# Kernel tuning notes

Measured on AMD Instinct MI355X. Metric: run time of the kernel, lower is better.

The kernel has to match this reference:

```python
import jax, jax.numpy as jnp
import numpy as np

EPS = 1e-08


def squash(x):
    # x: [..., D]; scale by ||x||^2/(1+||x||^2) and normalize by ||x||
    lengths2 = jnp.sum(x * x, axis=-1, keepdims=True)
    lengths = jnp.sqrt(lengths2)
    return x * (lengths2 / (1.0 + lengths2)) / (lengths + EPS)


def setup_inputs() -> dict:
    key = jax.random.key(0)
    k1, = jax.random.split(key, 1)
    B, G, S, O, D = 32, 8, 1152, 10, 16
    u_predict = jax.random.normal(k1, (B, G, S, O, D), dtype=jnp.float32)
    b_param = jnp.zeros((G, 1, S, O), dtype=jnp.float32)
    return {"u_predict": u_predict, "b_param": b_param, "n_iterations": 3}


def reference(u_predict, b_param, n_iterations):
    B, G, S, O, D = u_predict.shape
    # b: expand param (G,1,S,O) -> (G,B,S,O), permute -> (B,G,S,O)
    b = jnp.transpose(jnp.broadcast_to(b_param, (G, B, S, O)), (1, 0, 2, 3))
    v = None
    for r in range(n_iterations):
        c = jax.nn.softmax(b, axis=3)[..., None]          # [B,G,S,O,1]
        s = jnp.sum(c * u_predict, axis=2)                # [B,G,O,D]
        v = squash(s)                                     # [B,G,O,D]
        if r < n_iterations - 1:
            # agreement: dot(u_predict, v) over D
            b = b + jnp.sum(u_predict * v[:, :, None], axis=-1)  # [B,G,S,O]
    return jnp.sum(v, axis=1)                             # [B,O,D]
```

## Files before the change

### kernel.cpp

```cpp
#include <hip/hip_runtime.h>
#include <hip/hip_fp16.h>
#include <stdint.h>

#define NB 32
#define NG 8
#define NS 1152
#define NO 10
#define ND 16
#define EPSV 1e-8f

#define THREADS 512
#define GRPS (THREADS / 4)
#define NSTEPS (NS / GRPS)
#define UHROW (NO * 4)

typedef float f4v __attribute__((ext_vector_type(4)));

__global__ __launch_bounds__(THREADS)
void AgreementRouting_72988674228343_kernel(const float* __restrict__ u,
                                            const float* __restrict__ bparam,
                                            const int* __restrict__ n_iter_p,
                                            float* __restrict__ out,
                                            uint2* __restrict__ uh)
{
    __shared__ float  b_lds[NS * NO];
    __shared__ float4 sred[8][NO][4];
    __shared__ float4 v_lds[NO][4];

    const int tid  = threadIdx.x;
    const int bg   = blockIdx.x;
    const int g    = bg & 7;
    const int bb   = bg >> 3;
    const int wave = tid >> 6;
    const int lane = tid & 63;
    const int d4   = tid & 3;
    const int grp  = tid >> 2;

    const int n = n_iter_p[0];

    const float* bp = bparam + (size_t)g * (NS * NO);
    for (int i = tid; i < NS * NO; i += THREADS) b_lds[i] = bp[i];
    if (tid < NO * 4) v_lds[tid >> 2][tid & 3] = make_float4(0.f, 0.f, 0.f, 0.f);

    const f4v* ub  = (const f4v*)u + (size_t)bg * (NS * NO * 4);
    uint2*     uhb = uh + (size_t)bg * (NS * UHROW);

    __syncthreads();

    for (int r = 0; r < n; ++r) {
        float4 sacc[NO];
#pragma unroll
        for (int o = 0; o < NO; ++o) sacc[o] = make_float4(0.f, 0.f, 0.f, 0.f);

        for (int step = 0; step < NSTEPS; ++step) {
            const int s = step * GRPS + grp;
            float4 uu[NO];
            float bnew[NO];

            if (r == 0) {
                const f4v* row = ub + (size_t)s * (NO * 4) + d4;
                f4v t[NO];
#pragma unroll
                for (int o = 0; o < NO; ++o) t[o] = __builtin_nontemporal_load(row + o * 4);
                if (n > 1) {
                    uint2* wrow = uhb + (size_t)s * UHROW + d4;
#pragma unroll
                    for (int o = 0; o < NO; ++o) {
                        const __half2 lo = __floats2half2_rn(t[o].x, t[o].y);
                        const __half2 hi = __floats2half2_rn(t[o].z, t[o].w);
                        uint2 pk;
                        pk.x = __builtin_bit_cast(uint32_t, lo);
                        pk.y = __builtin_bit_cast(uint32_t, hi);
                        wrow[o * 4] = pk;
                    }
                }
#pragma unroll
                for (int o = 0; o < NO; ++o) {
                    uu[o] = make_float4(t[o].x, t[o].y, t[o].z, t[o].w);
                    bnew[o] = b_lds[s * NO + o];
                }
            } else {
                const uint2* row = uhb + (size_t)s * UHROW + d4;
                uint2 pk[NO];
#pragma unroll
                for (int o = 0; o < NO; ++o) pk[o] = row[o * 4];
#pragma unroll
                for (int o = 0; o < NO; ++o) {
                    const float2 a = __half22float2(__builtin_bit_cast(__half2, pk[o].x));
                    const float2 b = __half22float2(__builtin_bit_cast(__half2, pk[o].y));
                    uu[o] = make_float4(a.x, a.y, b.x, b.y);
                }
#pragma unroll
                for (int o = 0; o < NO; ++o) {
                    const float4 vc = v_lds[o][d4];
                    float p = uu[o].x * vc.x + uu[o].y * vc.y +
                              uu[o].z * vc.z + uu[o].w * vc.w;
                    p += __shfl_xor(p, 1);
                    p += __shfl_xor(p, 2);
                    bnew[o] = b_lds[s * NO + o] + p;
                }
            }

            float mx = bnew[0];
#pragma unroll
            for (int o = 1; o < NO; ++o) mx = fmaxf(mx, bnew[o]);
            float ss = 0.f;
#pragma unroll
            for (int o = 0; o < NO; ++o) { bnew[o] = __expf(bnew[o] - mx); ss += bnew[o]; }
            const float inv = 1.f / ss;
#pragma unroll
            for (int o = 0; o < NO; ++o) {
                const float c = bnew[o] * inv;
                sacc[o].x += c * uu[o].x;
                sacc[o].y += c * uu[o].y;
                sacc[o].z += c * uu[o].z;
                sacc[o].w += c * uu[o].w;
            }
        }

#pragma unroll
        for (int o = 0; o < NO; ++o) {
#pragma unroll
            for (int mask = 4; mask <= 32; mask <<= 1) {
                sacc[o].x += __shfl_xor(sacc[o].x, mask);
                sacc[o].y += __shfl_xor(sacc[o].y, mask);
                sacc[o].z += __shfl_xor(sacc[o].z, mask);
                sacc[o].w += __shfl_xor(sacc[o].w, mask);
            }
        }
        if (lane < 4) {
#pragma unroll
            for (int o = 0; o < NO; ++o) sred[wave][o][lane] = sacc[o];
        }
        __syncthreads();

        if (tid < NO * 4) {
            const int o = tid >> 2, dd = tid & 3;
            float4 sv = sred[0][o][dd];
#pragma unroll
            for (int w = 1; w < 8; ++w) {
                const float4 t = sred[w][o][dd];
                sv.x += t.x; sv.y += t.y; sv.z += t.z; sv.w += t.w;
            }
            float q = sv.x * sv.x + sv.y * sv.y + sv.z * sv.z + sv.w * sv.w;
            q += __shfl_xor(q, 1);
            q += __shfl_xor(q, 2);
            const float len = sqrtf(q);
            const float f = (q / (1.f + q)) / (len + EPSV);
            const float4 vv = make_float4(sv.x * f, sv.y * f, sv.z * f, sv.w * f);
            const float4 c4 = v_lds[o][dd];
            v_lds[o][dd] = make_float4(c4.x + vv.x, c4.y + vv.y,
                                       c4.z + vv.z, c4.w + vv.w);
            if (r == n - 1) {
                float* op = out + (size_t)bb * (NO * ND) + o * ND + dd * 4;
                atomicAdd(op + 0, vv.x);
                atomicAdd(op + 1, vv.y);
                atomicAdd(op + 2, vv.z);
                atomicAdd(op + 3, vv.w);
            }
        }
        __syncthreads();
    }
}

extern "C" void kernel_launch(void* const* d_in, const int* in_sizes, int n_in,
                              void* d_out, int out_size, void* d_ws, size_t ws_size,
                              hipStream_t stream) {
    const float* u   = (const float*)d_in[0];
    const float* bp  = (const float*)d_in[1];
    const int*   nit = (const int*)d_in[2];
    float* out = (float*)d_out;
    uint2* uh  = (uint2*)d_ws;

    hipMemsetAsync(out, 0, (size_t)out_size * sizeof(float), stream);

    AgreementRouting_72988674228343_kernel<<<dim3(NB * NG), dim3(THREADS), 0, stream>>>(
        u, bp, nit, out, uh);
}
```

Before: 313.2 us.

## Remap thread-to-data layout to 8-element chunks and software-prefetch fp16 rows

Each of the 4 threads per capsule row now owns contiguous 8-float chunks covering half of an output's D dimension for alternating outputs, instead of 4 floats across all 10 outputs. This lets the fp16 cache be written and read with 16-byte uint4 accesses and cuts shuffle traffic for the dot products. Later iterations fully unroll the S loop with double-buffered prefetch of the next row's loads, and v is held in registers. The cost is higher register pressure from the 5x8 accumulators, the prefetch buffers and the v copy, which may reduce occupancy.

```diff
diff --git a/kernel.cpp b/kernel.cpp
--- a/kernel.cpp
+++ b/kernel.cpp
@@ -10,9 +10,7 @@
 #define EPSV 1e-8f
 
 #define THREADS 512
-#define GRPS (THREADS / 4)
-#define NSTEPS (NS / GRPS)
-#define UHROW (NO * 4)
+#define NSTEPS 9
 
 typedef float f4v __attribute__((ext_vector_type(4)));
 
@@ -21,11 +19,11 @@
                                             const float* __restrict__ bparam,
                                             const int* __restrict__ n_iter_p,
                                             float* __restrict__ out,
-                                            uint2* __restrict__ uh)
+                                            uint4* __restrict__ uh)
 {
-    __shared__ float  b_lds[NS * NO];
-    __shared__ float4 sred[8][NO][4];
-    __shared__ float4 v_lds[NO][4];
+    __shared__ float b_lds[NS * NO];
+    __shared__ float sredl[8][4][5][8];
+    __shared__ float v_lds[NO * ND];
 
     const int tid  = threadIdx.x;
     const int bg   = blockIdx.x;
@@ -33,131 +31,162 @@
     const int bb   = bg >> 3;
     const int wave = tid >> 6;
     const int lane = tid & 63;
-    const int d4   = tid & 3;
-    const int grp  = tid >> 2;
+    const int j    = tid & 3;
+    const int rl   = tid >> 2;
+    const int half8 = j & 1;
+    const int par   = j >> 1;
 
     const int n = n_iter_p[0];
 
     const float* bp = bparam + (size_t)g * (NS * NO);
     for (int i = tid; i < NS * NO; i += THREADS) b_lds[i] = bp[i];
-    if (tid < NO * 4) v_lds[tid >> 2][tid & 3] = make_float4(0.f, 0.f, 0.f, 0.f);
-
-    const f4v* ub  = (const f4v*)u + (size_t)bg * (NS * NO * 4);
-    uint2*     uhb = uh + (size_t)bg * (NS * UHROW);
+    if (tid < NO * ND) v_lds[tid] = 0.f;
+
+    const f4v* u4  = (const f4v*)u + (size_t)bg * (NS * 40);
+    uint4*     uh4 = uh + (size_t)bg * (NS * 20);
 
     __syncthreads();
 
     for (int r = 0; r < n; ++r) {
-        float4 sacc[NO];
-#pragma unroll
-        for (int o = 0; o < NO; ++o) sacc[o] = make_float4(0.f, 0.f, 0.f, 0.f);
-
-        for (int step = 0; step < NSTEPS; ++step) {
-            const int s = step * GRPS + grp;
-            float4 uu[NO];
-            float bnew[NO];
-
-            if (r == 0) {
-                const f4v* row = ub + (size_t)s * (NO * 4) + d4;
-                f4v t[NO];
-#pragma unroll
-                for (int o = 0; o < NO; ++o) t[o] = __builtin_nontemporal_load(row + o * 4);
-                if (n > 1) {
-                    uint2* wrow = uhb + (size_t)s * UHROW + d4;
-#pragma unroll
-                    for (int o = 0; o < NO; ++o) {
-                        const __half2 lo = __floats2half2_rn(t[o].x, t[o].y);
-                        const __half2 hi = __floats2half2_rn(t[o].z, t[o].w);
-                        uint2 pk;
-                        pk.x = __builtin_bit_cast(uint32_t, lo);
-                        pk.y = __builtin_bit_cast(uint32_t, hi);
-                        wrow[o * 4] = pk;
+        float sacc[5][8];
+#pragma unroll
+        for (int k = 0; k < 5; ++k)
+#pragma unroll
+            for (int i = 0; i < 8; ++i) sacc[k][i] = 0.f;
+
+        if (r == 0) {
+            for (int step = 0; step < NSTEPS; ++step) {
+                const int s = step * 128 + rl;
+                float uf[5][8];
+#pragma unroll
+                for (int k = 0; k < 5; ++k) {
+                    const int f = k * 4 + j;
+                    const f4v a = __builtin_nontemporal_load(u4 + (size_t)s * 40 + f * 2);
+                    const f4v b = __builtin_nontemporal_load(u4 + (size_t)s * 40 + f * 2 + 1);
+                    uf[k][0] = a.x; uf[k][1] = a.y; uf[k][2] = a.z; uf[k][3] = a.w;
+                    uf[k][4] = b.x; uf[k][5] = b.y; uf[k][6] = b.z; uf[k][7] = b.w;
+                    if (n > 1) {
+                        uint4 pk;
+                        pk.x = __builtin_bit_cast(uint32_t, __floats2half2_rn(a.x, a.y));
+                        pk.y = __builtin_bit_cast(uint32_t, __floats2half2_rn(a.z, a.w));
+                        pk.z = __builtin_bit_cast(uint32_t, __floats2half2_rn(b.x, b.y));
+                        pk.w = __builtin_bit_cast(uint32_t, __floats2half2_rn(b.z, b.w));
+                        uh4[(size_t)s * 20 + f] = pk;
                     }
                 }
-#pragma unroll
-                for (int o = 0; o < NO; ++o) {
-                    uu[o] = make_float4(t[o].x, t[o].y, t[o].z, t[o].w);
-                    bnew[o] = b_lds[s * NO + o];
-                }
-            } else {
-                const uint2* row = uhb + (size_t)s * UHROW + d4;
-                uint2 pk[NO];
-#pragma unroll
-                for (int o = 0; o < NO; ++o) pk[o] = row[o * 4];
-#pragma unroll
-                for (int o = 0; o < NO; ++o) {
-                    const float2 a = __half22float2(__builtin_bit_cast(__half2, pk[o].x));
-                    const float2 b = __half22float2(__builtin_bit_cast(__half2, pk[o].y));
-                    uu[o] = make_float4(a.x, a.y, b.x, b.y);
-                }
-#pragma unroll
-                for (int o = 0; o < NO; ++o) {
-                    const float4 vc = v_lds[o][d4];
-                    float p = uu[o].x * vc.x + uu[o].y * vc.y +
-                              uu[o].z * vc.z + uu[o].w * vc.w;
+                float bn[NO];
+#pragma unroll
+                for (int o = 0; o < NO; ++o) bn[o] = b_lds[s * NO + o];
+                float mx = bn[0];
+#pragma unroll
+                for (int o = 1; o < NO; ++o) mx = fmaxf(mx, bn[o]);
+                float ss = 0.f;
+#pragma unroll
+                for (int o = 0; o < NO; ++o) { bn[o] = __expf(bn[o] - mx); ss += bn[o]; }
+                const float inv = 1.f / ss;
+#pragma unroll
+                for (int k = 0; k < 5; ++k) {
+                    const float c = bn[2 * k + par] * inv;
+#pragma unroll
+                    for (int i = 0; i < 8; ++i) sacc[k][i] += c * uf[k][i];
+                }
+            }
+        } else {
+            float vc[5][8];
+#pragma unroll
+            for (int k = 0; k < 5; ++k) {
+                const int o = 2 * k + par;
+#pragma unroll
+                for (int i = 0; i < 8; ++i) vc[k][i] = v_lds[o * ND + half8 * 8 + i];
+            }
+
+            uint4 ld[2][5];
+#pragma unroll
+            for (int k = 0; k < 5; ++k)
+                ld[0][k] = uh4[(size_t)rl * 20 + k * 4 + j];
+
+#pragma unroll
+            for (int step = 0; step < NSTEPS; ++step) {
+                const int cur = step & 1;
+                if (step + 1 < NSTEPS) {
+                    const int s2 = (step + 1) * 128 + rl;
+#pragma unroll
+                    for (int k = 0; k < 5; ++k)
+                        ld[cur ^ 1][k] = uh4[(size_t)s2 * 20 + k * 4 + j];
+                }
+                const int s = step * 128 + rl;
+                float uf[5][8];
+#pragma unroll
+                for (int k = 0; k < 5; ++k) {
+                    const float2 p0 = __half22float2(__builtin_bit_cast(__half2, ld[cur][k].x));
+                    const float2 p1 = __half22float2(__builtin_bit_cast(__half2, ld[cur][k].y));
+                    const float2 p2 = __half22float2(__builtin_bit_cast(__half2, ld[cur][k].z));
+                    const float2 p3 = __half22float2(__builtin_bit_cast(__half2, ld[cur][k].w));
+                    uf[k][0] = p0.x; uf[k][1] = p0.y; uf[k][2] = p1.x; uf[k][3] = p1.y;
+                    uf[k][4] = p2.x; uf[k][5] = p2.y; uf[k][6] = p3.x; uf[k][7] = p3.y;
+                }
+                float bo[5], bx[5];
+#pragma unroll
+                for (int k = 0; k < 5; ++k) {
+                    float p = 0.f;
+#pragma unroll
+                    for (int i = 0; i < 8; ++i) p += uf[k][i] * vc[k][i];
                     p += __shfl_xor(p, 1);
-                    p += __shfl_xor(p, 2);
-                    bnew[o] = b_lds[s * NO + o] + p;
-                }
-            }
-
-            float mx = bnew[0];
-#pragma unroll
-            for (int o = 1; o < NO; ++o) mx = fmaxf(mx, bnew[o]);
-            float ss = 0.f;
-#pragma unroll
-            for (int o = 0; o < NO; ++o) { bnew[o] = __expf(bnew[o] - mx); ss += bnew[o]; }
-            const float inv = 1.f / ss;
-#pragma unroll
-            for (int o = 0; o < NO; ++o) {
-                const float c = bnew[o] * inv;
-                sacc[o].x += c * uu[o].x;
-                sacc[o].y += c * uu[o].y;
-                sacc[o].z += c * uu[o].z;
-                sacc[o].w += c * uu[o].w;
+                    bo[k] = b_lds[s * NO + 2 * k + par] + p;
+                    bx[k] = __shfl_xor(bo[k], 2);
+                }
+                float mx = fmaxf(bo[0], bx[0]);
+#pragma unroll
+                for (int k = 1; k < 5; ++k) mx = fmaxf(mx, fmaxf(bo[k], bx[k]));
+                float ss = 0.f;
+                float eo[5];
+#pragma unroll
+                for (int k = 0; k < 5; ++k) {
+                    eo[k] = __expf(bo[k] - mx);
+                    ss += eo[k] + __expf(bx[k] - mx);
+                }
+                const float inv = 1.f / ss;
+#pragma unroll
+                for (int k = 0; k < 5; ++k) {
+                    const float c = eo[k] * inv;
+#pragma unroll
+                    for (int i = 0; i < 8; ++i) sacc[k][i] += c * uf[k][i];
+                }
             }
         }
 
 #pragma unroll
-        for (int o = 0; o < NO; ++o) {
-#pragma unroll
-            for (int mask = 4; mask <= 32; mask <<= 1) {
-                sacc[o].x += __shfl_xor(sacc[o].x, mask);
-                sacc[o].y += __shfl_xor(sacc[o].y, mask);
-                sacc[o].z += __shfl_xor(sacc[o].z, mask);
-                sacc[o].w += __shfl_xor(sacc[o].w, mask);
-            }
-        }
+        for (int k = 0; k < 5; ++k)
+#pragma unroll
+            for (int i = 0; i < 8; ++i) {
+#pragma unroll
+                for (int mask = 4; mask <= 32; mask <<= 1)
+                    sacc[k][i] += __shfl_xor(sacc[k][i], mask);
+            }
         if (lane < 4) {
 #pragma unroll
-            for (int o = 0; o < NO; ++o) sred[wave][o][lane] = sacc[o];
+            for (int k = 0; k < 5; ++k)
+#pragma unroll
+                for (int i = 0; i < 8; ++i) sredl[wave][lane][k][i] = sacc[k][i];
         }
         __syncthreads();
 
-        if (tid < NO * 4) {
-            const int o = tid >> 2, dd = tid & 3;
-            float4 sv = sred[0][o][dd];
-#pragma unroll
-            for (int w = 1; w < 8; ++w) {
-                const float4 t = sred[w][o][dd];
-                sv.x += t.x; sv.y += t.y; sv.z += t.z; sv.w += t.w;
-            }
-            float q = sv.x * sv.x + sv.y * sv.y + sv.z * sv.z + sv.w * sv.w;
-            q += __shfl_xor(q, 1);
-            q += __shfl_xor(q, 2);
+        if (tid < NO * ND) {
+            const int o = tid >> 4, d = tid & 15;
+            const int jj = (o & 1) * 2 + (d >> 3);
+            const int k  = o >> 1, i = d & 7;
+            float s = sredl[0][jj][k][i];
+#pragma unroll
+            for (int w = 1; w < 8; ++w) s += sredl[w][jj][k][i];
+            float q = s * s;
+            q += __shfl_xor(q, 1); q += __shfl_xor(q, 2);
+            q += __shfl_xor(q, 4); q += __shfl_xor(q, 8);
             const float len = sqrtf(q);
             const float f = (q / (1.f + q)) / (len + EPSV);
-            const float4 vv = make_float4(sv.x * f, sv.y * f, sv.z * f, sv.w * f);
-            const float4 c4 = v_lds[o][dd];
-            v_lds[o][dd] = make_float4(c4.x + vv.x, c4.y + vv.y,
-                                       c4.z + vv.z, c4.w + vv.w);
-            if (r == n - 1) {
-                float* op = out + (size_t)bb * (NO * ND) + o * ND + dd * 4;
-                atomicAdd(op + 0, vv.x);
-                atomicAdd(op + 1, vv.y);
-                atomicAdd(op + 2, vv.z);
-                atomicAdd(op + 3, vv.w);
-            }
+            const float v = s * f;
+            v_lds[tid] += v;
+            if (r == n - 1)
+                atomicAdd(&out[(size_t)bb * (NO * ND) + tid], v);
         }
         __syncthreads();
     }
@@ -170,7 +199,7 @@
     const float* bp  = (const float*)d_in[1];
     const int*   nit = (const int*)d_in[2];
     float* out = (float*)d_out;
-    uint2* uh  = (uint2*)d_ws;
+    uint4* uh  = (uint4*)d_ws;
 
     hipMemsetAsync(out, 0, (size_t)out_size * sizeof(float), stream);
 
```

After: 355.0 us. 1.13x slower.
